# Kernel tuning notes

Hardware: AMD Instinct MI355X
Metric: run time of the kernel (lower is better)

The kernel has to match this reference:

```python
import jax, jax.numpy as jnp
import numpy as np

V, K, C, F = 100000, 64, 3, 16
HID = [64, 64, 64]  # 'large' pca-net hidden widths (config.yaml stand-in)
EPS = 1e-4


def setup_inputs() -> dict:
    key = jax.random.key(0)
    ks = jax.random.split(key, 12)
    inp = {
        "coordinates": jax.random.normal(ks[0], (V, C), jnp.float32),
        "distsq": jax.random.uniform(ks[1], (V, K), jnp.float32),
        "features": jax.random.uniform(ks[2], (V, F), jnp.float32),
        "n_idxs": jax.random.randint(ks[3], (V, K), 0, V, jnp.int32),
    }
    dims = [C * C] + HID + [C * C]
    for i in range(len(dims) - 1):
        fan_in = dims[i]
        inp[f"W{i}"] = jax.random.normal(ks[4 + 2 * i], (dims[i], dims[i + 1]), jnp.float32) / np.sqrt(fan_in)
        inp[f"b{i}"] = jnp.zeros((dims[i + 1],), jnp.float32)
    return inp


def _neighbour_covariance(coordinates, distsq, features, n_idxs):
    # gather neighbour coords/features: [V,K,C], [V,K,F]
    nbc = jnp.take(coordinates, n_idxs, axis=0)
    nbf = jnp.take(features, n_idxs, axis=0)
    # per-neighbour per-feature weights, distsq pre-scaled by 10 in call()
    w = nbf * jnp.exp(-10.0 * distsq)[:, :, None]          # [V,K,F]
    wsum = jnp.sum(w, axis=1) + EPS                         # [V,F]
    mean = jnp.einsum("vkf,vkc->vfc", w, nbc) / wsum[:, :, None]  # [V,F,C]
    # E[x x^T] - mu mu^T (avoids materializing [V,K,F,C] centered diffs)
    m2 = jnp.einsum("vkf,vkc,vkd->vfcd", w, nbc, nbc) / wsum[:, :, None, None]
    cov = m2 - mean[:, :, :, None] * mean[:, :, None, :]    # [V,F,C,C]
    return cov, mean


def reference(coordinates, distsq, features, n_idxs,
              W0, b0, W1, b1, W2, b2, W3, b3):
    cov, mean = _neighbour_covariance(coordinates, distsq, features, n_idxs)
    x = cov.reshape(-1, C * C)                              # [V*F, C^2]
    # per-layer path: ELU on every layer, including the final one
    for Wl, bl in ((W0, b0), (W1, b1), (W2, b2), (W3, b3)):
        x = jax.nn.elu(x @ Wl + bl)
    return x.reshape(-1, F * C * C)                         # [V, F*C^2]
```

## Files before the change

### kernel.cpp

```cpp
#include <hip/hip_runtime.h>
#include <math.h>

#define NV 100000
#define NK 64
#define NF 16
#define EPS_W 1e-4f
#define WS_NEED ((size_t)NV * 16 * 32)

typedef __attribute__((ext_vector_type(8))) short bf16x8;
typedef __attribute__((ext_vector_type(4))) float f32x4;

__device__ __forceinline__ unsigned short bfu(float x) {
    return __builtin_bit_cast(unsigned short, (__bf16)x);
}
__device__ __forceinline__ unsigned int pk2(float lo, float hi) {
    return (unsigned int)bfu(lo) | ((unsigned int)bfu(hi) << 16);
}
__device__ __forceinline__ float eluf(float x) {
    return x > 0.f ? x : __expf(x) - 1.f;
}

__launch_bounds__(256)
__global__ void cov_kernel(const float* __restrict__ coords,
                           const float* __restrict__ distsq,
                           const float* __restrict__ feats,
                           const int*   __restrict__ nidx,
                           unsigned char* __restrict__ ws)
{
    __shared__ float sEW[16][64];
    __shared__ int   sIX[16][64];
    const int tid = threadIdx.x;
    const int gv  = tid >> 4;
    const int f   = tid & 15;
    const int v   = blockIdx.x * 16 + gv;

    {
        const size_t base = (size_t)v * NK + 4 * f;
        float4 d4 = *(const float4*)(distsq + base);
        int4   i4 = *(const int4*)(nidx + base);
        sEW[gv][4*f+0] = __expf(-10.f * d4.x);
        sEW[gv][4*f+1] = __expf(-10.f * d4.y);
        sEW[gv][4*f+2] = __expf(-10.f * d4.z);
        sEW[gv][4*f+3] = __expf(-10.f * d4.w);
        sIX[gv][4*f+0] = i4.x; sIX[gv][4*f+1] = i4.y;
        sIX[gv][4*f+2] = i4.z; sIX[gv][4*f+3] = i4.w;
    }
    __syncthreads();

    float s = 0.f, m0=0.f,m1=0.f,m2=0.f;
    float q00=0.f,q01=0.f,q02=0.f,q11=0.f,q12=0.f,q22=0.f;

    #pragma unroll 4
    for (int k = 0; k < NK; ++k) {
        int   idx = sIX[gv][k];
        float ew  = sEW[gv][k];
        float w   = feats[(size_t)idx * NF + f] * ew;
        float x = coords[(size_t)idx*3+0];
        float y = coords[(size_t)idx*3+1];
        float z = coords[(size_t)idx*3+2];
        s += w;
        m0 = fmaf(w,x,m0); m1 = fmaf(w,y,m1); m2 = fmaf(w,z,m2);
        float wx=w*x, wy=w*y, wz=w*z;
        q00=fmaf(wx,x,q00); q01=fmaf(wx,y,q01); q02=fmaf(wx,z,q02);
        q11=fmaf(wy,y,q11); q12=fmaf(wy,z,q12); q22=fmaf(wz,z,q22);
    }
    float inv = 1.f / (s + EPS_W);
    float mu0=m0*inv, mu1=m1*inv, mu2=m2*inv;
    float c00=fmaf(-mu0,mu0,q00*inv);
    float c01=fmaf(-mu0,mu1,q01*inv);
    float c02=fmaf(-mu0,mu2,q02*inv);
    float c11=fmaf(-mu1,mu1,q11*inv);
    float c12=fmaf(-mu1,mu2,q12*inv);
    float c22=fmaf(-mu2,mu2,q22*inv);

    uint4 lo, hi;
    lo.x = pk2(c00, c01);
    lo.y = pk2(c02, c01);
    lo.z = pk2(c11, c12);
    lo.w = pk2(c02, c12);
    hi.x = pk2(c22, 1.0f);
    hi.y = 0u; hi.z = 0u; hi.w = 0u;

    uint4* dst = (uint4*)(ws + ((size_t)v * 16 + f) * 32);
    dst[0] = lo;
    dst[1] = hi;
}

__device__ __forceinline__ bf16x8 rdfrag(const short* hb, int c, int g, int kc) {
    int boff = ((kc << 6) + (g << 4)) ^ ((c & 7) << 4);
    return *(const bf16x8*)(hb + c * 64 + (boff >> 1));
}
__device__ __forceinline__ void wrH(short* hb, int c, int g, int t,
                                    unsigned int p01, unsigned int p23) {
    int boff = ((t << 5) + (g << 3)) ^ ((c & 7) << 4);
    uint2 val; val.x = p01; val.y = p23;
    *(uint2*)(hb + c * 64 + (boff >> 1)) = val;
}
__device__ __forceinline__ bf16x8 rdW(const short* sw, int c, int g, int t, int kc) {
    int byte = (t << 11) + (c << 7) + (kc << 6) + (g << 4);
    byte ^= (c & 7) << 4;
    return *(const bf16x8*)((const char*)sw + byte);
}

__launch_bounds__(256)
__global__ void mlp3_kernel(const unsigned char* __restrict__ ws,
                            const float* __restrict__ W0, const float* __restrict__ b0,
                            const float* __restrict__ W1, const float* __restrict__ b1,
                            const float* __restrict__ W2, const float* __restrict__ b2,
                            const float* __restrict__ W3, const float* __restrict__ b3,
                            float* __restrict__ out)
{
    __shared__ __align__(16) short sW1[4096];
    __shared__ __align__(16) short sW2[4096];
    __shared__ float sB1[64], sB2[64], sB3[16];
    __shared__ __align__(16) short hbuf[4][2][1024];

    const int tid  = threadIdx.x;
    const int wid  = tid >> 6;
    const int lane = tid & 63;
    const int c    = lane & 15;
    const int g    = lane >> 4;

    union U8 { short s[8]; bf16x8 v; };

    #pragma unroll
    for (int r = 0; r < 2; ++r) {
        int t = tid + r * 256;
        int j = t & 63, o = t >> 6;
        U8 u1, u2;
        #pragma unroll
        for (int i = 0; i < 8; ++i) {
            u1.s[i] = (short)bfu(W1[(8 * o + i) * 64 + j]);
            u2.s[i] = (short)bfu(W2[(8 * o + i) * 64 + j]);
        }
        int byte = ((j << 7) + (o << 4)) ^ ((j & 7) << 4);
        *(bf16x8*)((char*)sW1 + byte) = u1.v;
        *(bf16x8*)((char*)sW2 + byte) = u2.v;
    }
    if (tid < 64) { sB1[tid] = b1[tid]; sB2[tid] = b2[tid]; }
    if (tid < 16) sB3[tid] = (tid < 9) ? b3[tid] : 0.f;
    __syncthreads();

    bf16x8 w0f[4], w3f[2];
    #pragma unroll
    for (int t = 0; t < 4; ++t) {
        U8 u;
        #pragma unroll
        for (int i = 0; i < 8; ++i) {
            int k = 8 * g + i;
            float val = 0.f;
            if (k < 9)       val = W0[k * 64 + 16 * t + c];
            else if (k == 9) val = b0[16 * t + c];
            u.s[i] = (short)bfu(val);
        }
        w0f[t] = u.v;
    }
    #pragma unroll
    for (int kc = 0; kc < 2; ++kc) {
        U8 u;
        #pragma unroll
        for (int i = 0; i < 8; ++i) {
            int k = 32 * kc + 8 * g + i;
            u.s[i] = (short)bfu(c < 9 ? W3[k * 9 + c] : 0.f);
        }
        w3f[kc] = u.v;
    }

    short* hb0 = &hbuf[wid][0][0];
    short* hb1 = &hbuf[wid][1][0];

    const int npair  = NV / 2;
    const int stride = gridDim.x * 4;
    for (int p = blockIdx.x * 4 + wid; p < npair; p += stride) {
        const int v0 = 2 * p, v1 = 2 * p + 1;
        f32x4 A0[4], A1[4];

        {
            bf16x8 bin0 = *(const bf16x8*)(ws + (size_t)v0 * 512 + (c << 5) + ((g & 1) << 4));
            bf16x8 bin1 = *(const bf16x8*)(ws + (size_t)v1 * 512 + (c << 5) + ((g & 1) << 4));
            #pragma unroll
            for (int t = 0; t < 4; ++t) {
                f32x4 z4 = {0.f, 0.f, 0.f, 0.f};
                A0[t] = __builtin_amdgcn_mfma_f32_16x16x32_bf16(w0f[t], bin0, z4, 0, 0, 0);
                A1[t] = __builtin_amdgcn_mfma_f32_16x16x32_bf16(w0f[t], bin1, z4, 0, 0, 0);
            }
            #pragma unroll
            for (int t = 0; t < 4; ++t) {
                wrH(hb0, c, g, t, pk2(eluf(A0[t][0]), eluf(A0[t][1])),
                                  pk2(eluf(A0[t][2]), eluf(A0[t][3])));
                wrH(hb1, c, g, t, pk2(eluf(A1[t][0]), eluf(A1[t][1])),
                                  pk2(eluf(A1[t][2]), eluf(A1[t][3])));
            }
        }
        __asm__ volatile("s_waitcnt lgkmcnt(0)" ::: "memory");

        {
            bf16x8 h00 = rdfrag(hb0, c, g, 0), h01 = rdfrag(hb0, c, g, 1);
            bf16x8 h10 = rdfrag(hb1, c, g, 0), h11 = rdfrag(hb1, c, g, 1);
            #pragma unroll
            for (int t = 0; t < 4; ++t) {
                bf16x8 wa = rdW(sW1, c, g, t, 0);
                bf16x8 wb = rdW(sW1, c, g, t, 1);
                f32x4 z4 = {0.f, 0.f, 0.f, 0.f};
                f32x4 a0 = __builtin_amdgcn_mfma_f32_16x16x32_bf16(wa, h00, z4, 0, 0, 0);
                a0       = __builtin_amdgcn_mfma_f32_16x16x32_bf16(wb, h01, a0, 0, 0, 0);
                f32x4 a1 = __builtin_amdgcn_mfma_f32_16x16x32_bf16(wa, h10, z4, 0, 0, 0);
                a1       = __builtin_amdgcn_mfma_f32_16x16x32_bf16(wb, h11, a1, 0, 0, 0);
                A0[t] = a0; A1[t] = a1;
            }
            #pragma unroll
            for (int t = 0; t < 4; ++t) {
                float4 bb = *(const float4*)(sB1 + 16 * t + 4 * g);
                wrH(hb0, c, g, t, pk2(eluf(A0[t][0] + bb.x), eluf(A0[t][1] + bb.y)),
                                  pk2(eluf(A0[t][2] + bb.z), eluf(A0[t][3] + bb.w)));
                wrH(hb1, c, g, t, pk2(eluf(A1[t][0] + bb.x), eluf(A1[t][1] + bb.y)),
                                  pk2(eluf(A1[t][2] + bb.z), eluf(A1[t][3] + bb.w)));
            }
        }
        __asm__ volatile("s_waitcnt lgkmcnt(0)" ::: "memory");

        {
            bf16x8 h00 = rdfrag(hb0, c, g, 0), h01 = rdfrag(hb0, c, g, 1);
            bf16x8 h10 = rdfrag(hb1, c, g, 0), h11 = rdfrag(hb1, c, g, 1);
            #pragma unroll
            for (int t = 0; t < 4; ++t) {
                bf16x8 wa = rdW(sW2, c, g, t, 0);
                bf16x8 wb = rdW(sW2, c, g, t, 1);
                f32x4 z4 = {0.f, 0.f, 0.f, 0.f};
                f32x4 a0 = __builtin_amdgcn_mfma_f32_16x16x32_bf16(wa, h00, z4, 0, 0, 0);
                a0       = __builtin_amdgcn_mfma_f32_16x16x32_bf16(wb, h01, a0, 0, 0, 0);
                f32x4 a1 = __builtin_amdgcn_mfma_f32_16x16x32_bf16(wa, h10, z4, 0, 0, 0);
                a1       = __builtin_amdgcn_mfma_f32_16x16x32_bf16(wb, h11, a1, 0, 0, 0);
                A0[t] = a0; A1[t] = a1;
            }
            #pragma unroll
            for (int t = 0; t < 4; ++t) {
                float4 bb = *(const float4*)(sB2 + 16 * t + 4 * g);
                wrH(hb0, c, g, t, pk2(eluf(A0[t][0] + bb.x), eluf(A0[t][1] + bb.y)),
                                  pk2(eluf(A0[t][2] + bb.z), eluf(A0[t][3] + bb.w)));
                wrH(hb1, c, g, t, pk2(eluf(A1[t][0] + bb.x), eluf(A1[t][1] + bb.y)),
                                  pk2(eluf(A1[t][2] + bb.z), eluf(A1[t][3] + bb.w)));
            }
        }
        __asm__ volatile("s_waitcnt lgkmcnt(0)" ::: "memory");

        {
            bf16x8 h00 = rdfrag(hb0, c, g, 0), h01 = rdfrag(hb0, c, g, 1);
            bf16x8 h10 = rdfrag(hb1, c, g, 0), h11 = rdfrag(hb1, c, g, 1);
            f32x4 z4 = {0.f, 0.f, 0.f, 0.f};
            f32x4 a0 = __builtin_amdgcn_mfma_f32_16x16x32_bf16(w3f[0], h00, z4, 0, 0, 0);
            a0       = __builtin_amdgcn_mfma_f32_16x16x32_bf16(w3f[1], h01, a0, 0, 0, 0);
            f32x4 a1 = __builtin_amdgcn_mfma_f32_16x16x32_bf16(w3f[0], h10, z4, 0, 0, 0);
            a1       = __builtin_amdgcn_mfma_f32_16x16x32_bf16(w3f[1], h11, a1, 0, 0, 0);
            float4 bb = *(const float4*)(sB3 + 4 * g);
            float* op0 = out + (size_t)(v0 * 16 + c) * 9 + (g << 2);
            float* op1 = out + (size_t)(v1 * 16 + c) * 9 + (g << 2);
            if (g < 2) {
                op0[0] = eluf(a0[0] + bb.x); op0[1] = eluf(a0[1] + bb.y);
                op0[2] = eluf(a0[2] + bb.z); op0[3] = eluf(a0[3] + bb.w);
                op1[0] = eluf(a1[0] + bb.x); op1[1] = eluf(a1[1] + bb.y);
                op1[2] = eluf(a1[2] + bb.z); op1[3] = eluf(a1[3] + bb.w);
            } else if (g == 2) {
                op0[0] = eluf(a0[0] + bb.x);
                op1[0] = eluf(a1[0] + bb.x);
            }
        }
    }
}

__launch_bounds__(256, 2)
__global__ void fused_pca_mlp(const float* __restrict__ coords,
                              const float* __restrict__ distsq,
                              const float* __restrict__ feats,
                              const int*   __restrict__ nidx,
                              const float* __restrict__ W0, const float* __restrict__ b0,
                              const float* __restrict__ W1, const float* __restrict__ b1,
                              const float* __restrict__ W2, const float* __restrict__ b2,
                              const float* __restrict__ W3, const float* __restrict__ b3,
                              float* __restrict__ out)
{
    __shared__ __align__(16) float sW0t[64 * 9];
    __shared__ __align__(16) float sW1t[64 * 64];
    __shared__ __align__(16) float sW2t[64 * 64];
    __shared__ __align__(16) float sW3t[9 * 64];
    __shared__ float sB0[64], sB1[64], sB2[64], sB3[9];
    const int tid = threadIdx.x;
    for (int t = tid; t < 64 * 9; t += 256) { int j = t / 9, i = t - j * 9; sW0t[t] = W0[i * 64 + j]; }
    for (int t = tid; t < 64 * 64; t += 256) { int j = t >> 6, i = t & 63; sW1t[t] = W1[i * 64 + j]; }
    for (int t = tid; t < 64 * 64; t += 256) { int j = t >> 6, i = t & 63; sW2t[t] = W2[i * 64 + j]; }
    for (int t = tid; t < 9 * 64; t += 256) { int j = t >> 6, i = t & 63; sW3t[t] = W3[i * 9 + j]; }
    if (tid < 64) { sB0[tid] = b0[tid]; sB1[tid] = b1[tid]; sB2[tid] = b2[tid]; }
    if (tid < 9)  { sB3[tid] = b3[tid]; }
    __syncthreads();
    const int g = tid >> 4, f = tid & 15;
    const int v = blockIdx.x * 16 + g;
    if (v >= NV) return;
    const int* nix = nidx + (size_t)v * NK;
    const float* dsq = distsq + (size_t)v * NK;
    float s = 0.f, m0=0,m1=0,m2=0, q00=0,q01=0,q02=0,q11=0,q12=0,q22=0;
    #pragma unroll 4
    for (int k = 0; k < NK; ++k) {
        int idx = nix[k];
        float ew = __expf(-10.0f * dsq[k]);
        float w = feats[(size_t)idx * NF + f] * ew;
        float x = coords[(size_t)idx*3+0], y = coords[(size_t)idx*3+1], z = coords[(size_t)idx*3+2];
        s += w; m0 = fmaf(w,x,m0); m1 = fmaf(w,y,m1); m2 = fmaf(w,z,m2);
        float wx=w*x, wy=w*y, wz=w*z;
        q00=fmaf(wx,x,q00); q01=fmaf(wx,y,q01); q02=fmaf(wx,z,q02);
        q11=fmaf(wy,y,q11); q12=fmaf(wy,z,q12); q22=fmaf(wz,z,q22);
    }
    float inv = 1.0f/(s+EPS_W), mu0=m0*inv, mu1=m1*inv, mu2=m2*inv;
    float xr[9];
    xr[0]=fmaf(-mu0,mu0,q00*inv); xr[1]=fmaf(-mu0,mu1,q01*inv); xr[2]=fmaf(-mu0,mu2,q02*inv);
    xr[3]=xr[1]; xr[4]=fmaf(-mu1,mu1,q11*inv); xr[5]=fmaf(-mu1,mu2,q12*inv);
    xr[6]=xr[2]; xr[7]=xr[5]; xr[8]=fmaf(-mu2,mu2,q22*inv);
    float h[64], gg[64];
    #pragma unroll
    for (int j = 0; j < 64; ++j) {
        float aa = sB0[j]; const float* wr = sW0t + j * 9;
        #pragma unroll
        for (int i = 0; i < 9; ++i) aa = fmaf(xr[i], wr[i], aa);
        h[j] = eluf(aa);
    }
    #pragma unroll
    for (int j = 0; j < 64; ++j) {
        float aa = sB1[j]; const float4* wr = (const float4*)(sW1t + (j << 6));
        #pragma unroll
        for (int i4 = 0; i4 < 16; ++i4) { float4 wv = wr[i4];
            aa = fmaf(h[4*i4+0],wv.x,aa); aa = fmaf(h[4*i4+1],wv.y,aa);
            aa = fmaf(h[4*i4+2],wv.z,aa); aa = fmaf(h[4*i4+3],wv.w,aa); }
        gg[j] = eluf(aa);
    }
    #pragma unroll
    for (int j = 0; j < 64; ++j) {
        float aa = sB2[j]; const float4* wr = (const float4*)(sW2t + (j << 6));
        #pragma unroll
        for (int i4 = 0; i4 < 16; ++i4) { float4 wv = wr[i4];
            aa = fmaf(gg[4*i4+0],wv.x,aa); aa = fmaf(gg[4*i4+1],wv.y,aa);
            aa = fmaf(gg[4*i4+2],wv.z,aa); aa = fmaf(gg[4*i4+3],wv.w,aa); }
        h[j] = eluf(aa);
    }
    float o[9];
    #pragma unroll
    for (int j = 0; j < 9; ++j) {
        float aa = sB3[j]; const float4* wr = (const float4*)(sW3t + (j << 6));
        #pragma unroll
        for (int i4 = 0; i4 < 16; ++i4) { float4 wv = wr[i4];
            aa = fmaf(h[4*i4+0],wv.x,aa); aa = fmaf(h[4*i4+1],wv.y,aa);
            aa = fmaf(h[4*i4+2],wv.z,aa); aa = fmaf(h[4*i4+3],wv.w,aa); }
        o[j] = eluf(aa);
    }
    float* op = out + ((size_t)v * NF + f) * 9;
    #pragma unroll
    for (int j = 0; j < 9; ++j) op[j] = o[j];
}

extern "C" void kernel_launch(void* const* d_in, const int* in_sizes, int n_in,
                              void* d_out, int out_size, void* d_ws, size_t ws_size,
                              hipStream_t stream) {
    (void)in_sizes; (void)n_in; (void)out_size;
    const float* coords = (const float*)d_in[0];
    const float* distsq = (const float*)d_in[1];
    const float* feats  = (const float*)d_in[2];
    const int*   nidx   = (const int*)d_in[3];
    const float* W0 = (const float*)d_in[4];
    const float* b0 = (const float*)d_in[5];
    const float* W1 = (const float*)d_in[6];
    const float* b1 = (const float*)d_in[7];
    const float* W2 = (const float*)d_in[8];
    const float* b2 = (const float*)d_in[9];
    const float* W3 = (const float*)d_in[10];
    const float* b3 = (const float*)d_in[11];
    float* out = (float*)d_out;

    if (ws_size >= WS_NEED) {
        unsigned char* ws = (unsigned char*)d_ws;
        hipLaunchKernelGGL(cov_kernel, dim3(NV / 16), dim3(256), 0, stream,
                           coords, distsq, feats, nidx, ws);
        hipLaunchKernelGGL(mlp3_kernel, dim3(2048), dim3(256), 0, stream,
                           ws, W0, b0, W1, b1, W2, b2, W3, b3, out);
    } else {
        hipLaunchKernelGGL(fused_pca_mlp, dim3(NV / 16), dim3(256), 0, stream,
                           coords, distsq, feats, nidx,
                           W0, b0, W1, b1, W2, b2, W3, b3, out);
    }
}
```

Measured before the change: 200.7 us.

## Pad coords to float4, prefetch MLP inputs, fold biases into MFMA accumulators

A new prep kernel packs the xyz coordinates into float4 so the covariance gather does one 16-byte load per neighbour instead of three scalar loads, and that loop's unroll goes from 4 to 8. The MLP kernel prefetches the next pair's input fragments while the current pair computes. It also seeds the MFMA accumulators with the biases held in registers, dropping the shared-memory bias reads and adds. Smaller changes are a packed bf16x2 conversion intrinsic and a grid size of 2084. The extra prep launch and the larger workspace add overhead and register pressure.

```diff
diff --git a/kernel.cpp b/kernel.cpp
--- a/kernel.cpp
+++ b/kernel.cpp
@@ -1,11 +1,16 @@
 #include <hip/hip_runtime.h>
+#include <hip/hip_bf16.h>
 #include <math.h>
 
 #define NV 100000
 #define NK 64
 #define NF 16
 #define EPS_W 1e-4f
-#define WS_NEED ((size_t)NV * 16 * 32)
+#define ROWS_BYTES ((size_t)NV * 16 * 32)
+#define C4_BYTES   ((size_t)NV * 16)
+#define WS_NEED    ROWS_BYTES
+#define WS_NEED_C4 (ROWS_BYTES + C4_BYTES)
+#define GRID_MLP 2084
 
 typedef __attribute__((ext_vector_type(8))) short bf16x8;
 typedef __attribute__((ext_vector_type(4))) float f32x4;
@@ -14,14 +19,32 @@
     return __builtin_bit_cast(unsigned short, (__bf16)x);
 }
 __device__ __forceinline__ unsigned int pk2(float lo, float hi) {
-    return (unsigned int)bfu(lo) | ((unsigned int)bfu(hi) << 16);
+    float2 t; t.x = lo; t.y = hi;
+    __hip_bfloat162 r = __float22bfloat162_rn(t);
+    unsigned int u;
+    __builtin_memcpy(&u, &r, 4);
+    return u;
 }
 __device__ __forceinline__ float eluf(float x) {
     return x > 0.f ? x : __expf(x) - 1.f;
 }
 
+__global__ void prep_kernel(const float* __restrict__ coords, float4* __restrict__ c4) {
+    int v = blockIdx.x * 256 + threadIdx.x;
+    if (v < NV) {
+        float4 r;
+        r.x = coords[3 * v + 0];
+        r.y = coords[3 * v + 1];
+        r.z = coords[3 * v + 2];
+        r.w = 0.f;
+        c4[v] = r;
+    }
+}
+
+template<bool C4>
 __launch_bounds__(256)
 __global__ void cov_kernel(const float* __restrict__ coords,
+                           const float4* __restrict__ c4,
                            const float* __restrict__ distsq,
                            const float* __restrict__ feats,
                            const int*   __restrict__ nidx,
@@ -50,14 +73,20 @@
     float s = 0.f, m0=0.f,m1=0.f,m2=0.f;
     float q00=0.f,q01=0.f,q02=0.f,q11=0.f,q12=0.f,q22=0.f;
 
-    #pragma unroll 4
+    #pragma unroll 8
     for (int k = 0; k < NK; ++k) {
         int   idx = sIX[gv][k];
         float ew  = sEW[gv][k];
         float w   = feats[(size_t)idx * NF + f] * ew;
-        float x = coords[(size_t)idx*3+0];
-        float y = coords[(size_t)idx*3+1];
-        float z = coords[(size_t)idx*3+2];
+        float x, y, z;
+        if constexpr (C4) {
+            float4 cd = c4[idx];
+            x = cd.x; y = cd.y; z = cd.z;
+        } else {
+            x = coords[(size_t)idx*3+0];
+            y = coords[(size_t)idx*3+1];
+            z = coords[(size_t)idx*3+2];
+        }
         s += w;
         m0 = fmaf(w,x,m0); m1 = fmaf(w,y,m1); m2 = fmaf(w,z,m2);
         float wx=w*x, wy=w*y, wz=w*z;
@@ -103,7 +132,7 @@
 }
 
 __launch_bounds__(256)
-__global__ void mlp3_kernel(const unsigned char* __restrict__ ws,
+__global__ void mlp4_kernel(const unsigned char* __restrict__ ws,
                             const float* __restrict__ W0, const float* __restrict__ b0,
                             const float* __restrict__ W1, const float* __restrict__ b1,
                             const float* __restrict__ W2, const float* __restrict__ b2,
@@ -112,7 +141,6 @@
 {
     __shared__ __align__(16) short sW1[4096];
     __shared__ __align__(16) short sW2[4096];
-    __shared__ float sB1[64], sB2[64], sB3[16];
     __shared__ __align__(16) short hbuf[4][2][1024];
 
     const int tid  = threadIdx.x;
@@ -137,8 +165,6 @@
         *(bf16x8*)((char*)sW1 + byte) = u1.v;
         *(bf16x8*)((char*)sW2 + byte) = u2.v;
     }
-    if (tid < 64) { sB1[tid] = b1[tid]; sB2[tid] = b2[tid]; }
-    if (tid < 16) sB3[tid] = (tid < 9) ? b3[tid] : 0.f;
     __syncthreads();
 
     bf16x8 w0f[4], w3f[2];
@@ -165,19 +191,42 @@
         }
         w3f[kc] = u.v;
     }
+    float b1v[16], b2v[16], b3v[4];
+    #pragma unroll
+    for (int t = 0; t < 4; ++t)
+        #pragma unroll
+        for (int r = 0; r < 4; ++r) {
+            b1v[4 * t + r] = b1[16 * t + 4 * g + r];
+            b2v[4 * t + r] = b2[16 * t + 4 * g + r];
+        }
+    #pragma unroll
+    for (int r = 0; r < 4; ++r)
+        b3v[r] = (4 * g + r < 9) ? b3[4 * g + r] : 0.f;
 
     short* hb0 = &hbuf[wid][0][0];
     short* hb1 = &hbuf[wid][1][0];
 
     const int npair  = NV / 2;
     const int stride = gridDim.x * 4;
-    for (int p = blockIdx.x * 4 + wid; p < npair; p += stride) {
-        const int v0 = 2 * p, v1 = 2 * p + 1;
+    int p = blockIdx.x * 4 + wid;
+    if (p >= npair) return;
+
+    const unsigned char* wp = ws + (size_t)p * 1024 + (c << 5) + ((g & 1) << 4);
+    const size_t wstep = (size_t)stride * 1024;
+    float* op0 = out + (size_t)p * 288 + 9 * c + (g << 2);
+    const size_t ostep = (size_t)stride * 288;
+
+    bf16x8 bin0 = *(const bf16x8*)(wp);
+    bf16x8 bin1 = *(const bf16x8*)(wp + 512);
+
+    for (; p < npair; p += stride) {
+        const unsigned char* wpn = (p + stride < npair) ? (wp + wstep) : wp;
+        bf16x8 nb0 = *(const bf16x8*)(wpn);
+        bf16x8 nb1 = *(const bf16x8*)(wpn + 512);
+
         f32x4 A0[4], A1[4];
 
         {
-            bf16x8 bin0 = *(const bf16x8*)(ws + (size_t)v0 * 512 + (c << 5) + ((g & 1) << 4));
-            bf16x8 bin1 = *(const bf16x8*)(ws + (size_t)v1 * 512 + (c << 5) + ((g & 1) << 4));
             #pragma unroll
             for (int t = 0; t < 4; ++t) {
                 f32x4 z4 = {0.f, 0.f, 0.f, 0.f};
@@ -201,20 +250,20 @@
             for (int t = 0; t < 4; ++t) {
                 bf16x8 wa = rdW(sW1, c, g, t, 0);
                 bf16x8 wb = rdW(sW1, c, g, t, 1);
-                f32x4 z4 = {0.f, 0.f, 0.f, 0.f};
-                f32x4 a0 = __builtin_amdgcn_mfma_f32_16x16x32_bf16(wa, h00, z4, 0, 0, 0);
-                a0       = __builtin_amdgcn_mfma_f32_16x16x32_bf16(wb, h01, a0, 0, 0, 0);
-                f32x4 a1 = __builtin_amdgcn_mfma_f32_16x16x32_bf16(wa, h10, z4, 0, 0, 0);
-                a1       = __builtin_amdgcn_mfma_f32_16x16x32_bf16(wb, h11, a1, 0, 0, 0);
+                f32x4 a0 = { b1v[4*t+0], b1v[4*t+1], b1v[4*t+2], b1v[4*t+3] };
+                f32x4 a1 = a0;
+                a0 = __builtin_amdgcn_mfma_f32_16x16x32_bf16(wa, h00, a0, 0, 0, 0);
+                a0 = __builtin_amdgcn_mfma_f32_16x16x32_bf16(wb, h01, a0, 0, 0, 0);
+                a1 = __builtin_amdgcn_mfma_f32_16x16x32_bf16(wa, h10, a1, 0, 0, 0);
+                a1 = __builtin_amdgcn_mfma_f32_16x16x32_bf16(wb, h11, a1, 0, 0, 0);
                 A0[t] = a0; A1[t] = a1;
             }
             #pragma unroll
             for (int t = 0; t < 4; ++t) {
-                float4 bb = *(const float4*)(sB1 + 16 * t + 4 * g);
-                wrH(hb0, c, g, t, pk2(eluf(A0[t][0] + bb.x), eluf(A0[t][1] + bb.y)),
-                                  pk2(eluf(A0[t][2] + bb.z), eluf(A0[t][3] + bb.w)));
-                wrH(hb1, c, g, t, pk2(eluf(A1[t][0] + bb.x), eluf(A1[t][1] + bb.y)),
-                                  pk2(eluf(A1[t][2] + bb.z), eluf(A1[t][3] + bb.w)));
+                wrH(hb0, c, g, t, pk2(eluf(A0[t][0]), eluf(A0[t][1])),
+                                  pk2(eluf(A0[t][2]), eluf(A0[t][3])));
+                wrH(hb1, c, g, t, pk2(eluf(A1[t][0]), eluf(A1[t][1])),
+                                  pk2(eluf(A1[t][2]), eluf(A1[t][3])));
             }
         }
         __asm__ volatile("s_waitcnt lgkmcnt(0)" ::: "memory");
@@ -226,20 +275,20 @@
             for (int t = 0; t < 4; ++t) {
                 bf16x8 wa = rdW(sW2, c, g, t, 0);
                 bf16x8 wb = rdW(sW2, c, g, t, 1);
-                f32x4 z4 = {0.f, 0.f, 0.f, 0.f};
-                f32x4 a0 = __builtin_amdgcn_mfma_f32_16x16x32_bf16(wa, h00, z4, 0, 0, 0);
-                a0       = __builtin_amdgcn_mfma_f32_16x16x32_bf16(wb, h01, a0, 0, 0, 0);
-                f32x4 a1 = __builtin_amdgcn_mfma_f32_16x16x32_bf16(wa, h10, z4, 0, 0, 0);
-                a1       = __builtin_amdgcn_mfma_f32_16x16x32_bf16(wb, h11, a1, 0, 0, 0);
+                f32x4 a0 = { b2v[4*t+0], b2v[4*t+1], b2v[4*t+2], b2v[4*t+3] };
+                f32x4 a1 = a0;
+                a0 = __builtin_amdgcn_mfma_f32_16x16x32_bf16(wa, h00, a0, 0, 0, 0);
+                a0 = __builtin_amdgcn_mfma_f32_16x16x32_bf16(wb, h01, a0, 0, 0, 0);
+                a1 = __builtin_amdgcn_mfma_f32_16x16x32_bf16(wa, h10, a1, 0, 0, 0);
+                a1 = __builtin_amdgcn_mfma_f32_16x16x32_bf16(wb, h11, a1, 0, 0, 0);
                 A0[t] = a0; A1[t] = a1;
             }
             #pragma unroll
             for (int t = 0; t < 4; ++t) {
-                float4 bb = *(const float4*)(sB2 + 16 * t + 4 * g);
-                wrH(hb0, c, g, t, pk2(eluf(A0[t][0] + bb.x), eluf(A0[t][1] + bb.y)),
-                                  pk2(eluf(A0[t][2] + bb.z), eluf(A0[t][3] + bb.w)));
-                wrH(hb1, c, g, t, pk2(eluf(A1[t][0] + bb.x), eluf(A1[t][1] + bb.y)),
-                                  pk2(eluf(A1[t][2] + bb.z), eluf(A1[t][3] + bb.w)));
+                wrH(hb0, c, g, t, pk2(eluf(A0[t][0]), eluf(A0[t][1])),
+                                  pk2(eluf(A0[t][2]), eluf(A0[t][3])));
+                wrH(hb1, c, g, t, pk2(eluf(A1[t][0]), eluf(A1[t][1])),
+                                  pk2(eluf(A1[t][2]), eluf(A1[t][3])));
             }
         }
         __asm__ volatile("s_waitcnt lgkmcnt(0)" ::: "memory");
@@ -247,24 +296,27 @@
         {
             bf16x8 h00 = rdfrag(hb0, c, g, 0), h01 = rdfrag(hb0, c, g, 1);
             bf16x8 h10 = rdfrag(hb1, c, g, 0), h11 = rdfrag(hb1, c, g, 1);
-            f32x4 z4 = {0.f, 0.f, 0.f, 0.f};
-            f32x4 a0 = __builtin_amdgcn_mfma_f32_16x16x32_bf16(w3f[0], h00, z4, 0, 0, 0);
-            a0       = __builtin_amdgcn_mfma_f32_16x16x32_bf16(w3f[1], h01, a0, 0, 0, 0);
-            f32x4 a1 = __builtin_amdgcn_mfma_f32_16x16x32_bf16(w3f[0], h10, z4, 0, 0, 0);
-            a1       = __builtin_amdgcn_mfma_f32_16x16x32_bf16(w3f[1], h11, a1, 0, 0, 0);
-            float4 bb = *(const float4*)(sB3 + 4 * g);
-            float* op0 = out + (size_t)(v0 * 16 + c) * 9 + (g << 2);
-            float* op1 = out + (size_t)(v1 * 16 + c) * 9 + (g << 2);
+            f32x4 a0 = { b3v[0], b3v[1], b3v[2], b3v[3] };
+            f32x4 a1 = a0;
+            a0 = __builtin_amdgcn_mfma_f32_16x16x32_bf16(w3f[0], h00, a0, 0, 0, 0);
+            a0 = __builtin_amdgcn_mfma_f32_16x16x32_bf16(w3f[1], h01, a0, 0, 0, 0);
+            a1 = __builtin_amdgcn_mfma_f32_16x16x32_bf16(w3f[0], h10, a1, 0, 0, 0);
+            a1 = __builtin_amdgcn_mfma_f32_16x16x32_bf16(w3f[1], h11, a1, 0, 0, 0);
+            float* op1 = op0 + 144;
             if (g < 2) {
-                op0[0] = eluf(a0[0] + bb.x); op0[1] = eluf(a0[1] + bb.y);
-                op0[2] = eluf(a0[2] + bb.z); op0[3] = eluf(a0[3] + bb.w);
-                op1[0] = eluf(a1[0] + bb.x); op1[1] = eluf(a1[1] + bb.y);
-                op1[2] = eluf(a1[2] + bb.z); op1[3] = eluf(a1[3] + bb.w);
+                op0[0] = eluf(a0[0]); op0[1] = eluf(a0[1]);
+                op0[2] = eluf(a0[2]); op0[3] = eluf(a0[3]);
+                op1[0] = eluf(a1[0]); op1[1] = eluf(a1[1]);
+                op1[2] = eluf(a1[2]); op1[3] = eluf(a1[3]);
             } else if (g == 2) {
-                op0[0] = eluf(a0[0] + bb.x);
-                op1[0] = eluf(a1[0] + bb.x);
-            }
-        }
+                op0[0] = eluf(a0[0]);
+                op1[0] = eluf(a1[0]);
+            }
+        }
+
+        bin0 = nb0; bin1 = nb1;
+        wp = wpn;
+        op0 += ostep;
     }
 }
 
@@ -373,11 +425,20 @@
     const float* b3 = (const float*)d_in[11];
     float* out = (float*)d_out;
 
-    if (ws_size >= WS_NEED) {
+    if (ws_size >= WS_NEED_C4) {
         unsigned char* ws = (unsigned char*)d_ws;
-        hipLaunchKernelGGL(cov_kernel, dim3(NV / 16), dim3(256), 0, stream,
-                           coords, distsq, feats, nidx, ws);
-        hipLaunchKernelGGL(mlp3_kernel, dim3(2048), dim3(256), 0, stream,
+        float4* c4 = (float4*)(ws + ROWS_BYTES);
+        hipLaunchKernelGGL(prep_kernel, dim3((NV + 255) / 256), dim3(256), 0, stream,
+                           coords, c4);
+        hipLaunchKernelGGL((cov_kernel<true>), dim3(NV / 16), dim3(256), 0, stream,
+                           coords, c4, distsq, feats, nidx, ws);
+        hipLaunchKernelGGL(mlp4_kernel, dim3(GRID_MLP), dim3(256), 0, stream,
+                           ws, W0, b0, W1, b1, W2, b2, W3, b3, out);
+    } else if (ws_size >= WS_NEED) {
+        unsigned char* ws = (unsigned char*)d_ws;
+        hipLaunchKernelGGL((cov_kernel<false>), dim3(NV / 16), dim3(256), 0, stream,
+                           coords, (const float4*)nullptr, distsq, feats, nidx, ws);
+        hipLaunchKernelGGL(mlp4_kernel, dim3(GRID_MLP), dim3(256), 0, stream,
                            ws, W0, b0, W1, b1, W2, b2, W3, b3, out);
     } else {
         hipLaunchKernelGGL(fused_pca_mlp, dim3(NV / 16), dim3(256), 0, stream,
```

New measurement: 220.4 us. 9.8% more time.
